# Optimization experiments

Hardware: AMD Instinct MI355X
Metric: run time of the kernel (lower is better)

## Reference

```python
import jax, jax.numpy as jnp
import numpy as np

N, C, H, W = 4, 64, 64, 64
K = 3


def _unfold(x, k):
    """torch F.unfold with padding k//2: [n,c,h,w] -> [n, c*k*k, h*w].
    Feature ordering matches torch: index = c*k*k + i*k + j."""
    p = k // 2
    n, c, h, w = x.shape
    xp = jnp.pad(x, ((0, 0), (0, 0), (p, p), (p, p)))
    patches = jnp.stack(
        [xp[:, :, i:i + h, j:j + w] for i in range(k) for j in range(k)], axis=2
    )  # [n, c, k*k, h, w]
    return patches.reshape(n, c * k * k, h * w)


def _mask_vec(c, k):
    # causal patch mask from __init__: zero out center-and-right of middle row and all rows below
    m = np.ones((c, k, k), np.float32)
    m[:, k // 2, k // 2:] = 0
    m[:, k // 2 + 1:, :] = 0
    return jnp.asarray(m.reshape(1, c * k * k, 1))


def setup_inputs() -> dict:
    key = jax.random.key(0)
    k1, k2 = jax.random.split(key)
    y_hat = jax.random.normal(k1, (N, C, H, W), dtype=jnp.float32)
    y_prob = jax.random.uniform(k2, (N, 1, H, W), dtype=jnp.float32)
    return {"y_hat": y_hat, "y_prob": y_prob}


def reference(y_hat, y_prob):
    k = K
    n, c, h, w = y_hat.shape
    L = h * w
    mask = _mask_vec(c, k)

    u = _unfold(y_hat, k) * mask                              # [n, c*k*k, L]
    u = u / jnp.maximum(jnp.linalg.norm(u, axis=1, keepdims=True), 1e-12)
    R = jnp.einsum('nfl,nfm->nlm', u, u)                      # [n, L, L] cosine sims

    # eval path: keep strictly-upper triangle (causal: l < m)
    row = jnp.arange(L)[:, None]
    col = jnp.arange(L)[None, :]
    R = jnp.where(col > row, R, 0.0)

    R_star = jnp.max(R, axis=1)                               # [n, L]
    arg = jnp.argmax(R, axis=1).astype(jnp.int32)             # [n, L]

    y_unf = _unfold(y_hat, k)                                 # [n, c*k*k, L]
    ref_unfold = jnp.take_along_axis(y_unf, arg[:, None, :], axis=2)

    prob_unf = y_prob.reshape(n, -1, L)                       # 1x1 unfold
    U_unf = jnp.take_along_axis(prob_unf, arg[:, None, :], axis=2)

    S = R_star.reshape(n, 1, h, w)
    U = U_unf.reshape(n, -1, h, w)

    # eval-mode position-0 overrides
    S = S.at[:, :, 0, 0].set(1e-8)
    U = U.at[:, :, 0, 0].set(1e-8)
    ref_unfold = ref_unfold.at[:, :, 0].set(0.0)
    arg = arg.at[:, 0].set(-1)

    S = jnp.clip(S, 1e-8, 1.0)
    U = jnp.clip(U, 1e-8, 1.0)
    return S, U, ref_unfold, arg
```

## Files before the change

### kernel.cpp

```cpp
#include <hip/hip_runtime.h>
#include <stdint.h>

#define Nn 4
#define Cc 64
#define LL 4096
#define KK 256
#define TRI2 528

typedef _Float16 half8 __attribute__((ext_vector_type(8)));
typedef float f32x16 __attribute__((ext_vector_type(16)));
typedef float f4a __attribute__((ext_vector_type(4), aligned(4)));

__device__ __forceinline__ unsigned f2ord(float f) {
    unsigned u = __float_as_uint(f);
    return u ^ ((u & 0x80000000u) ? 0xFFFFFFFFu : 0x80000000u);
}
__device__ __forceinline__ float ord2f(unsigned o) {
    unsigned u = (o & 0x80000000u) ? (o ^ 0x80000000u) : ~o;
    return __uint_as_float(u);
}
__device__ __forceinline__ unsigned short h2u(_Float16 h) {
    union { _Float16 f; unsigned short u; } x; x.f = h; return x.u;
}

__global__ __launch_bounds__(256) void build_v(const float* __restrict__ yhat,
                                               unsigned short* __restrict__ VhT,
                                               unsigned short* __restrict__ VlT,
                                               unsigned long long* __restrict__ best) {
    int blk = blockIdx.x;
    int xcd = blk & 7;
    int n = xcd >> 1;
    int i64 = (blk >> 3) + (xcd & 1) * 128;
    int tid = threadIdx.x;
    if (tid < 16) best[(size_t)n * LL + i64 * 16 + tid] = 0ull;

    int cg = tid & 15;
    int l = i64 * 16 + (tid >> 4);
    int y = l >> 6, x = l & 63;
    const float* src = yhat + (size_t)n * (Cc * LL);

    float vals[16];
    float sumsq = 0.f;
#pragma unroll
    for (int ci = 0; ci < 4; ++ci) {
        const float* p = src + (cg * 4 + ci) * LL;
        float t0 = (y > 0 && x > 0)  ? p[l - 65] : 0.f;
        float t1 = (y > 0)           ? p[l - 64] : 0.f;
        float t2 = (y > 0 && x < 63) ? p[l - 63] : 0.f;
        float t3 = (x > 0)           ? p[l - 1]  : 0.f;
        vals[ci * 4 + 0] = t0; vals[ci * 4 + 1] = t1;
        vals[ci * 4 + 2] = t2; vals[ci * 4 + 3] = t3;
        sumsq += t0 * t0 + t1 * t1 + t2 * t2 + t3 * t3;
    }
    sumsq += __shfl_xor(sumsq, 1, 64);
    sumsq += __shfl_xor(sumsq, 2, 64);
    sumsq += __shfl_xor(sumsq, 4, 64);
    sumsq += __shfl_xor(sumsq, 8, 64);
    float inv = 1.f / fmaxf(sqrtf(sumsq), 1e-12f);

    size_t nl = (size_t)n * LL + l;
    unsigned short* dh = VhT + nl * KK + cg * 16;
    unsigned short* dl = VlT + nl * KK + cg * 16;
#pragma unroll
    for (int ci = 0; ci < 4; ++ci) {
        ushort4 hv, lv;
        unsigned short* ph = &hv.x;
        unsigned short* pl = &lv.x;
#pragma unroll
        for (int tp = 0; tp < 4; ++tp) {
            float v = vals[ci * 4 + tp] * inv;
            _Float16 h = (fabsf(v) < 6.1035e-5f) ? (_Float16)0 : (_Float16)v;
            _Float16 lo = (_Float16)((v - (float)h) * 2048.0f);
            ph[tp] = h2u(h * (_Float16)2048.0f);
            pl[tp] = h2u(lo);
        }
        *(ushort4*)(dh + ci * 4) = hv;
        *(ushort4*)(dl + ci * 4) = lv;
    }
}

__global__ __launch_bounds__(256) void simmax(const unsigned short* __restrict__ Vh,
                                              const unsigned short* __restrict__ Vl,
                                              unsigned long long* __restrict__ best) {
    __shared__ __align__(16) unsigned short S[16384];

    int bx = blockIdx.x;
    int xcd = bx & 7, idx = bx >> 3;
    int n = xcd >> 1;
    int t = (xcd & 1) * 264 + idx;
    int j = (int)((sqrtf(8.f * (float)t + 1.f) - 1.f) * 0.5f);
    while ((j + 1) * (j + 2) / 2 <= t) ++j;
    while (j * (j + 1) / 2 > t) --j;
    int i = t - j * (j + 1) / 2;
    int l0 = i * 128, m0 = j * 128;

    const unsigned short* VhB = Vh + (size_t)n * (LL * KK);
    const unsigned short* VlB = Vl + (size_t)n * (LL * KK);

    int tid = threadIdx.x;
    int w = tid >> 6, lane = tid & 63;
    int r5 = lane & 31, h5 = lane >> 5;
    int rw = (w & 1) * 64;
    int cw = (w >> 1) * 64;
    bool skip = (i == j) && (rw == 64) && (cw == 0);

    f32x16 acc[2][2];
#pragma unroll
    for (int r = 0; r < 2; ++r)
#pragma unroll
        for (int c = 0; c < 2; ++c) acc[r][c] = (f32x16)0.f;

    int srow = tid >> 2;
    int scl = tid & 3;
    int sp = (scl ^ ((srow >> 1) & 3)) * 8;
    int shg = scl * 8;

    int sfr = (r5 >> 1) & 3;

    for (int k0 = 0; k0 < KK; k0 += 32) {
        const size_t ra = (size_t)(l0 + srow) * KK + k0 + shg;
        const size_t rb = (size_t)(l0 + 64 + srow) * KK + k0 + shg;
        const size_t rc = (size_t)(m0 + srow) * KK + k0 + shg;
        const size_t rd = (size_t)(m0 + 64 + srow) * KK + k0 + shg;
        uint4 ah0 = *(const uint4*)(VhB + ra);
        uint4 ah1 = *(const uint4*)(VhB + rb);
        uint4 al0 = *(const uint4*)(VlB + ra);
        uint4 al1 = *(const uint4*)(VlB + rb);
        uint4 bh0 = *(const uint4*)(VhB + rc);
        uint4 bh1 = *(const uint4*)(VhB + rd);
        uint4 bl0 = *(const uint4*)(VlB + rc);
        uint4 bl1 = *(const uint4*)(VlB + rd);
        __syncthreads();
        *(uint4*)&S[srow * 32 + sp]                 = ah0;
        *(uint4*)&S[(64 + srow) * 32 + sp]          = ah1;
        *(uint4*)&S[4096 + srow * 32 + sp]          = al0;
        *(uint4*)&S[4096 + (64 + srow) * 32 + sp]   = al1;
        *(uint4*)&S[8192 + srow * 32 + sp]          = bh0;
        *(uint4*)&S[8192 + (64 + srow) * 32 + sp]   = bh1;
        *(uint4*)&S[12288 + srow * 32 + sp]         = bl0;
        *(uint4*)&S[12288 + (64 + srow) * 32 + sp]  = bl1;
        __syncthreads();
        if (!skip) {
            half8 fah[2][2], fal[2][2], fbh[2][2], fbl[2][2];
#pragma unroll
            for (int r = 0; r < 2; ++r)
#pragma unroll
                for (int kc = 0; kc < 2; ++kc) {
                    int pc = ((kc * 2 + h5) ^ sfr) * 8;
                    int ao = (rw + r * 32 + r5) * 32 + pc;
                    int bo = (cw + r * 32 + r5) * 32 + pc;
                    fah[r][kc] = *(half8*)&S[ao];
                    fal[r][kc] = *(half8*)&S[4096 + ao];
                    fbh[r][kc] = *(half8*)&S[8192 + bo];
                    fbl[r][kc] = *(half8*)&S[12288 + bo];
                }
#pragma unroll
            for (int kc = 0; kc < 2; ++kc)
#pragma unroll
                for (int r = 0; r < 2; ++r)
#pragma unroll
                    for (int c = 0; c < 2; ++c)
                        acc[r][c] = __builtin_amdgcn_mfma_f32_32x32x16_f16(fal[r][kc], fbh[c][kc], acc[r][c], 0, 0, 0);
#pragma unroll
            for (int kc = 0; kc < 2; ++kc)
#pragma unroll
                for (int r = 0; r < 2; ++r)
#pragma unroll
                    for (int c = 0; c < 2; ++c)
                        acc[r][c] = __builtin_amdgcn_mfma_f32_32x32x16_f16(fah[r][kc], fbl[c][kc], acc[r][c], 0, 0, 0);
#pragma unroll
            for (int kc = 0; kc < 2; ++kc)
#pragma unroll
                for (int r = 0; r < 2; ++r)
#pragma unroll
                    for (int c = 0; c < 2; ++c)
                        acc[r][c] = __builtin_amdgcn_mfma_f32_32x32x16_f16(fah[r][kc], fbh[c][kc], acc[r][c], 0, 0, 0);
        }
    }

    if (skip) return;
    unsigned long long* bb = best + (size_t)n * LL;
    const float s = 1.f / 4194304.f;
#pragma unroll
    for (int c = 0; c < 2; ++c) {
        int m = m0 + cw + c * 32 + r5;
        unsigned long long key = 0ull;
#pragma unroll
        for (int r = 0; r < 2; ++r)
#pragma unroll
            for (int g = 0; g < 16; ++g) {
                int l = l0 + rw + r * 32 + (g & 3) + 8 * (g >> 2) + 4 * h5;
                if (l < m) {
                    float v = acc[r][c][g] * s;
                    unsigned long long k2 =
                        ((unsigned long long)f2ord(v) << 32) |
                        (unsigned long long)(0xFFFFFFFFu - (unsigned)l);
                    key = (k2 > key) ? k2 : key;
                }
            }
        unsigned long long o = __shfl_xor(key, 32, 64);
        key = (o > key) ? o : key;
        if (h5 == 0 && key != 0ull) atomicMax(bb + m, key);
    }
}

__global__ __launch_bounds__(256) void writeout(const float* __restrict__ yhat,
                                                const float* __restrict__ yprob,
                                                const unsigned long long* __restrict__ best,
                                                float* __restrict__ out) {
    int blk = blockIdx.x;
    int xcd = blk & 7;
    int n = xcd >> 1;
    int idx = (blk >> 3) + (xcd & 1) * 512;
    int mb = idx >> 4;
    int fc = idx & 15;
    int tid = threadIdx.x;
    int mm = tid & 63;
    int fs = tid >> 6;
    int c = fc * 4 + fs;
    int m = mb * 64 + mm;

    unsigned long long key = best[(size_t)n * LL + m];
    unsigned l = 0xFFFFFFFFu - (unsigned)(key & 0xFFFFFFFFull);
    float val = ord2f((unsigned)(key >> 32));
    bool zero = (m == 0);
    if (zero) l = 0;
    int ly = (int)(l >> 6), lx = (int)(l & 63);

    float* Sout = out;
    float* Uout = out + 16384;
    float* Rout = out + 32768;
    float* Aout = out + 9469952;

    if (fc == 0 && fs == 0) {
        float S = zero ? 1e-8f : fminf(fmaxf(val, 1e-8f), 1.0f);
        float U = zero ? 1e-8f : fminf(fmaxf(yprob[(size_t)n * LL + l], 1e-8f), 1.0f);
        Sout[(size_t)n * LL + m] = S;
        Uout[(size_t)n * LL + m] = U;
        Aout[(size_t)n * LL + m] = zero ? -1.0f : (float)l;
    }

    const float* src = yhat + (size_t)n * (Cc * LL);
    const float* plane = src + (size_t)c * LL;
    float* dst = Rout + (size_t)n * (576 * LL) + m;
    bool fast = (!zero) && (lx >= 1) && (lx <= 61);
#pragma unroll
    for (int r3 = 0; r3 < 3; ++r3) {
        int yy = ly + r3 - 1;
        bool rowok = (!zero) && (yy >= 0) && (yy < 64);
        float t0 = 0.f, t1 = 0.f, t2 = 0.f;
        if (rowok) {
            if (fast) {
                f4a v = *(const f4a*)(plane + yy * 64 + lx - 1);
                t0 = v.x; t1 = v.y; t2 = v.z;
            } else {
                if (lx > 0)  t0 = plane[yy * 64 + lx - 1];
                t1 = plane[yy * 64 + lx];
                if (lx < 63) t2 = plane[yy * 64 + lx + 1];
            }
        }
        size_t f = (size_t)(c * 9 + r3 * 3) * LL;
        __builtin_nontemporal_store(t0, dst + f);
        __builtin_nontemporal_store(t1, dst + f + LL);
        __builtin_nontemporal_store(t2, dst + f + 2 * (size_t)LL);
    }
}

extern "C" void kernel_launch(void* const* d_in, const int* in_sizes, int n_in,
                              void* d_out, int out_size, void* d_ws, size_t ws_size,
                              hipStream_t stream) {
    const float* yhat  = (const float*)d_in[0];
    const float* yprob = (const float*)d_in[1];
    float* out = (float*)d_out;

    unsigned short* VhT = (unsigned short*)d_ws;
    unsigned short* VlT = (unsigned short*)((char*)d_ws + 8388608);
    unsigned long long* best =
        (unsigned long long*)((char*)d_ws + 16777216);

    build_v<<<1024, 256, 0, stream>>>(yhat, VhT, VlT, best);
    simmax<<<Nn * TRI2, 256, 0, stream>>>(VhT, VlT, best);
    writeout<<<4096, 256, 0, stream>>>(yhat, yprob, best, out);
}
```

Baseline: 156.1 us.

## Load MFMA fragments directly from global memory, dropping LDS staging and barriers

Removes the shared-memory tile and both per-iteration __syncthreads. Each wave now loads its half8 MFMA operand fragments straight from global memory through precomputed row pointers, and the main loop is unrolled by two. The skipped diagonal wave can exit early because no barriers remain. The cost is that each row is fetched once per wave instead of once per block, roughly doubling global/L2 traffic, and the per-lane loads are strided by row and less coalesced.

Measured after the change: 225.3 us. +44.3%, slower.

```diff
diff --git a/kernel.cpp b/kernel.cpp
--- a/kernel.cpp
+++ b/kernel.cpp
@@ -82,8 +82,6 @@
 __global__ __launch_bounds__(256) void simmax(const unsigned short* __restrict__ Vh,
                                               const unsigned short* __restrict__ Vl,
                                               unsigned long long* __restrict__ best) {
-    __shared__ __align__(16) unsigned short S[16384];
-
     int bx = blockIdx.x;
     int xcd = bx & 7, idx = bx >> 3;
     int n = xcd >> 1;
@@ -94,15 +92,24 @@
     int i = t - j * (j + 1) / 2;
     int l0 = i * 128, m0 = j * 128;
 
-    const unsigned short* VhB = Vh + (size_t)n * (LL * KK);
-    const unsigned short* VlB = Vl + (size_t)n * (LL * KK);
-
     int tid = threadIdx.x;
     int w = tid >> 6, lane = tid & 63;
     int r5 = lane & 31, h5 = lane >> 5;
     int rw = (w & 1) * 64;
     int cw = (w >> 1) * 64;
-    bool skip = (i == j) && (rw == 64) && (cw == 0);
+    if ((i == j) && (rw == 64) && (cw == 0)) return;
+
+    const unsigned short* VhB = Vh + (size_t)n * (LL * KK);
+    const unsigned short* VlB = Vl + (size_t)n * (LL * KK);
+
+    const unsigned short* pah[2], *pal[2], *pbh[2], *pbl[2];
+#pragma unroll
+    for (int r = 0; r < 2; ++r) {
+        size_t ar = (size_t)(l0 + rw + r * 32 + r5) * KK + h5 * 8;
+        size_t br = (size_t)(m0 + cw + r * 32 + r5) * KK + h5 * 8;
+        pah[r] = VhB + ar; pal[r] = VlB + ar;
+        pbh[r] = VhB + br; pbl[r] = VlB + br;
+    }
 
     f32x16 acc[2][2];
 #pragma unroll
@@ -110,75 +117,42 @@
 #pragma unroll
         for (int c = 0; c < 2; ++c) acc[r][c] = (f32x16)0.f;
 
-    int srow = tid >> 2;
-    int scl = tid & 3;
-    int sp = (scl ^ ((srow >> 1) & 3)) * 8;
-    int shg = scl * 8;
-
-    int sfr = (r5 >> 1) & 3;
-
+#pragma unroll 2
     for (int k0 = 0; k0 < KK; k0 += 32) {
-        const size_t ra = (size_t)(l0 + srow) * KK + k0 + shg;
-        const size_t rb = (size_t)(l0 + 64 + srow) * KK + k0 + shg;
-        const size_t rc = (size_t)(m0 + srow) * KK + k0 + shg;
-        const size_t rd = (size_t)(m0 + 64 + srow) * KK + k0 + shg;
-        uint4 ah0 = *(const uint4*)(VhB + ra);
-        uint4 ah1 = *(const uint4*)(VhB + rb);
-        uint4 al0 = *(const uint4*)(VlB + ra);
-        uint4 al1 = *(const uint4*)(VlB + rb);
-        uint4 bh0 = *(const uint4*)(VhB + rc);
-        uint4 bh1 = *(const uint4*)(VhB + rd);
-        uint4 bl0 = *(const uint4*)(VlB + rc);
-        uint4 bl1 = *(const uint4*)(VlB + rd);
-        __syncthreads();
-        *(uint4*)&S[srow * 32 + sp]                 = ah0;
-        *(uint4*)&S[(64 + srow) * 32 + sp]          = ah1;
-        *(uint4*)&S[4096 + srow * 32 + sp]          = al0;
-        *(uint4*)&S[4096 + (64 + srow) * 32 + sp]   = al1;
-        *(uint4*)&S[8192 + srow * 32 + sp]          = bh0;
-        *(uint4*)&S[8192 + (64 + srow) * 32 + sp]   = bh1;
-        *(uint4*)&S[12288 + srow * 32 + sp]         = bl0;
-        *(uint4*)&S[12288 + (64 + srow) * 32 + sp]  = bl1;
-        __syncthreads();
-        if (!skip) {
-            half8 fah[2][2], fal[2][2], fbh[2][2], fbl[2][2];
+        half8 fah[2][2], fal[2][2], fbh[2][2], fbl[2][2];
+#pragma unroll
+        for (int r = 0; r < 2; ++r)
+#pragma unroll
+            for (int kc = 0; kc < 2; ++kc) {
+                int off = k0 + kc * 16;
+                fah[r][kc] = *(const half8*)(pah[r] + off);
+                fal[r][kc] = *(const half8*)(pal[r] + off);
+                fbh[r][kc] = *(const half8*)(pbh[r] + off);
+                fbl[r][kc] = *(const half8*)(pbl[r] + off);
+            }
+#pragma unroll
+        for (int kc = 0; kc < 2; ++kc)
 #pragma unroll
             for (int r = 0; r < 2; ++r)
 #pragma unroll
-                for (int kc = 0; kc < 2; ++kc) {
-                    int pc = ((kc * 2 + h5) ^ sfr) * 8;
-                    int ao = (rw + r * 32 + r5) * 32 + pc;
-                    int bo = (cw + r * 32 + r5) * 32 + pc;
-                    fah[r][kc] = *(half8*)&S[ao];
-                    fal[r][kc] = *(half8*)&S[4096 + ao];
-                    fbh[r][kc] = *(half8*)&S[8192 + bo];
-                    fbl[r][kc] = *(half8*)&S[12288 + bo];
-                }
-#pragma unroll
-            for (int kc = 0; kc < 2; ++kc)
-#pragma unroll
-                for (int r = 0; r < 2; ++r)
-#pragma unroll
-                    for (int c = 0; c < 2; ++c)
-                        acc[r][c] = __builtin_amdgcn_mfma_f32_32x32x16_f16(fal[r][kc], fbh[c][kc], acc[r][c], 0, 0, 0);
-#pragma unroll
-            for (int kc = 0; kc < 2; ++kc)
-#pragma unroll
-                for (int r = 0; r < 2; ++r)
-#pragma unroll
-                    for (int c = 0; c < 2; ++c)
-                        acc[r][c] = __builtin_amdgcn_mfma_f32_32x32x16_f16(fah[r][kc], fbl[c][kc], acc[r][c], 0, 0, 0);
-#pragma unroll
-            for (int kc = 0; kc < 2; ++kc)
-#pragma unroll
-                for (int r = 0; r < 2; ++r)
-#pragma unroll
-                    for (int c = 0; c < 2; ++c)
-                        acc[r][c] = __builtin_amdgcn_mfma_f32_32x32x16_f16(fah[r][kc], fbh[c][kc], acc[r][c], 0, 0, 0);
-        }
-    }
-
-    if (skip) return;
+                for (int c = 0; c < 2; ++c)
+                    acc[r][c] = __builtin_amdgcn_mfma_f32_32x32x16_f16(fal[r][kc], fbh[c][kc], acc[r][c], 0, 0, 0);
+#pragma unroll
+        for (int kc = 0; kc < 2; ++kc)
+#pragma unroll
+            for (int r = 0; r < 2; ++r)
+#pragma unroll
+                for (int c = 0; c < 2; ++c)
+                    acc[r][c] = __builtin_amdgcn_mfma_f32_32x32x16_f16(fah[r][kc], fbl[c][kc], acc[r][c], 0, 0, 0);
+#pragma unroll
+        for (int kc = 0; kc < 2; ++kc)
+#pragma unroll
+            for (int r = 0; r < 2; ++r)
+#pragma unroll
+                for (int c = 0; c < 2; ++c)
+                    acc[r][c] = __builtin_amdgcn_mfma_f32_32x32x16_f16(fah[r][kc], fbh[c][kc], acc[r][c], 0, 0, 0);
+    }
+
     unsigned long long* bb = best + (size_t)n * LL;
     const float s = 1.f / 4194304.f;
 #pragma unroll
```
